# Kernel tuning notes

Hardware: AMD Instinct MI355X
Metric: run time of the kernel (lower is better)

Reference implementation:

```python
import jax, jax.numpy as jnp
import numpy as np

B = 8
C = 256
NS = [16384, 4096, 1024, 256, 1]  # point-pyramid sizes per level
D = 3                              # coordinate dim
EPS = (1e-06, 1e-06, 1e-06, 1e-06, 1e-06)


def _pm_level(x, coords_c, coords_n, idx, p_i, eps_i):
    """One hierarchical gather-weighted power-mean pooling step.
    x: (B, C, N)  coords_c: (B, N, D)  coords_n: (B, Nn, D)  idx: (B, N) in [0, Nn).
    Returns pooled features (B, C, Nn)."""
    Bq, Cq, N = x.shape
    Nn = coords_n.shape[1]
    Dd = coords_c.shape[-1]
    # gather parent coords for each child, delta to parent
    cn = jnp.take_along_axis(coords_n, idx[:, :, None], axis=1)            # (B,N,D)
    delta = coords_c - cn                                                   # (B,N,D)
    # per-parent max/min of delta (scatter_max / scatter_min)
    smax = jax.vmap(lambda d, ix: jax.ops.segment_max(d, ix, num_segments=Nn))(delta, idx)
    smin = jax.vmap(lambda d, ix: jax.ops.segment_min(d, ix, num_segments=Nn))(delta, idx)
    pos_ub = jnp.maximum(smax, 0.0)   # clamp(min=0)
    neg_lb = jnp.minimum(smin, 0.0)   # clamp(max=0)
    # gather bounds back to children, pick by sign of delta
    pos_g = jnp.take_along_axis(pos_ub, idx[:, :, None], axis=1)
    neg_g = jnp.take_along_axis(neg_lb, idx[:, :, None], axis=1)
    inuse = jnp.where(delta >= 0.0, pos_g, neg_g)
    w = 1.0 - jnp.abs(delta) / (jnp.abs(inuse) + 1e-6)                      # (B,N,D)
    # split channels across the D coordinate weights: [q, q, ..., q+r]
    q, r = Cq // Dd, Cq % Dd
    reps = np.asarray([q] * (Dd - 1) + [q + r])
    w_c = jnp.repeat(w, reps, axis=-1, total_repeat_length=Cq)              # (B,N,C)
    x_pow = jnp.maximum(x, eps_i) ** p_i                                    # (B,C,N)
    xw = x_pow.transpose(0, 2, 1) * w_c                                     # (B,N,C)
    # scatter_sum of weighted powers and of weights, per parent cell
    xw_s = jax.vmap(lambda a, ix: jax.ops.segment_sum(a, ix, num_segments=Nn))(xw, idx)   # (B,Nn,C)
    w_s = jax.vmap(lambda a, ix: jax.ops.segment_sum(a, ix, num_segments=Nn))(w_c, idx)   # (B,Nn,C)
    nxt = (xw_s / (w_s + 1e-6)) ** (1.0 / p_i)
    return nxt.transpose(0, 2, 1)                                           # (B,C,Nn)


def setup_inputs() -> dict:
    key = jax.random.key(0)
    ks = jax.random.split(key, 16)
    x = jax.random.normal(ks[0], (B, C, NS[0]), dtype=jnp.float32)
    coords = [jax.random.normal(ks[1 + i], (B, NS[i], D), dtype=jnp.float32) for i in range(5)]
    idxs = []
    for i in range(4):
        # every parent gets ~NS[i]/NS[i+1] children; permute per batch for irregular access
        base = jnp.arange(NS[i], dtype=jnp.int32) % NS[i + 1]
        bk = jax.random.split(ks[6 + i], B)
        idxs.append(jax.vmap(lambda k: jax.random.permutation(k, base))(bk))
    p = jnp.full((5,), 3.0, dtype=jnp.float32)
    return {"x": x,
            "idx0": idxs[0], "idx1": idxs[1], "idx2": idxs[2], "idx3": idxs[3],
            "coords0": coords[0], "coords1": coords[1], "coords2": coords[2],
            "coords3": coords[3], "coords4": coords[4],
            "p": p}


def reference(x, idx0, idx1, idx2, idx3, coords0, coords1, coords2, coords3, coords4, p):
    idxs = (idx0, idx1, idx2, idx3)
    coords = (coords0, coords1, coords2, coords3, coords4)
    cur = x
    for i in range(4):
        cur = _pm_level(cur, coords[i], coords[i + 1], idxs[i], p[i], EPS[i])
    return cur[..., 0]  # squeeze (B,C,1) -> (B,C)
```

## Files before the change

kernel.cpp:

```cpp
#include <hip/hip_runtime.h>
#include <math.h>

constexpr int B  = 8;
constexpr int C  = 256;
constexpr int Q  = 85;
constexpr int NS0 = 16384, NS1 = 4096, NS2 = 1024, NS3 = 256;
constexpr int PAR = NS1 + NS2 + NS3;
constexpr int SLT = NS0 + NS1 + NS2;

__device__ __forceinline__ int cdim(int c) {
    int d = c / Q;
    return d > 2 ? 2 : d;
}

__global__ void invert_fused_kernel(const int* __restrict__ idx0,
                                    const int* __restrict__ idx1,
                                    const int* __restrict__ idx2,
                                    const float* __restrict__ c0,
                                    const float* __restrict__ c1,
                                    const float* __restrict__ c2,
                                    const float* __restrict__ c3,
                                    const float* __restrict__ c4,
                                    unsigned* __restrict__ cnt,
                                    float4*   __restrict__ dslot,
                                    float*    __restrict__ w3,
                                    float*    __restrict__ z4) {
    __shared__ float sm[3][256];
    __shared__ float sn[3][256];

    if (blockIdx.y == 3) {
        if (blockIdx.x >= 8) return;
        int b = blockIdx.x;
        int n = threadIdx.x;

        float pc0 = c4[b * 3 + 0], pc1 = c4[b * 3 + 1], pc2 = c4[b * 3 + 2];
        const float* cp = &c3[((size_t)(b * 256 + n)) * 3];
        float d0 = cp[0] - pc0, d1 = cp[1] - pc1, d2 = cp[2] - pc2;
        sm[0][n] = d0; sm[1][n] = d1; sm[2][n] = d2;
        sn[0][n] = d0; sn[1][n] = d1; sn[2][n] = d2;
        __syncthreads();
        for (int s = 128; s > 0; s >>= 1) {
            if (n < s) {
#pragma unroll
                for (int d = 0; d < 3; ++d) {
                    sm[d][n] = fmaxf(sm[d][n], sm[d][n + s]);
                    sn[d][n] = fminf(sn[d][n], sn[d][n + s]);
                }
            }
            __syncthreads();
        }
        float pos0 = fmaxf(sm[0][0], 0.f), pos1 = fmaxf(sm[1][0], 0.f), pos2 = fmaxf(sm[2][0], 0.f);
        float neg0 = fminf(sn[0][0], 0.f), neg1 = fminf(sn[1][0], 0.f), neg2 = fminf(sn[2][0], 0.f);
        __syncthreads();

        float w0 = 1.f - fabsf(d0) / (fabsf(d0 >= 0.f ? pos0 : neg0) + 1e-6f);
        float w1 = 1.f - fabsf(d1) / (fabsf(d1 >= 0.f ? pos1 : neg1) + 1e-6f);
        float w2 = 1.f - fabsf(d2) / (fabsf(d2 >= 0.f ? pos2 : neg2) + 1e-6f);
        float* wp = &w3[((size_t)(b * 256 + n)) * 3];
        wp[0] = w0; wp[1] = w1; wp[2] = w2;

        sm[0][n] = w0; sm[1][n] = w1; sm[2][n] = w2;
        __syncthreads();
        for (int s = 128; s > 0; s >>= 1) {
            if (n < s) {
#pragma unroll
                for (int d = 0; d < 3; ++d) sm[d][n] += sm[d][n + s];
            }
            __syncthreads();
        }
        if (n == 0) {
            z4[b * 3 + 0] = sm[0][0];
            z4[b * 3 + 1] = sm[1][0];
            z4[b * 3 + 2] = sm[2][0];
        }
        return;
    }

    int lvl = blockIdx.y;
    const int*   idx = (lvl == 0) ? idx0 : (lvl == 1 ? idx1 : idx2);
    const float* cc  = (lvl == 0) ? c0   : (lvl == 1 ? c1   : c2);
    const float* cn  = (lvl == 0) ? c1   : (lvl == 1 ? c2   : c3);
    int N  = (lvl == 0) ? NS0 : (lvl == 1 ? NS1 : NS2);
    int Nn = (lvl == 0) ? NS1 : (lvl == 1 ? NS2 : NS3);
    int cbase = (lvl == 0) ? 0 : (lvl == 1 ? NS1 : NS1 + NS2);
    int sbase = (lvl == 0) ? 0 : (lvl == 1 ? NS0 : NS0 + NS1);

    int t = blockIdx.x * blockDim.x + threadIdx.x;
    if (t >= B * N) return;
    int b = t / N;
    int n = t - b * N;
    int j = idx[t];
    int pj = b * Nn + j;

    unsigned o = atomicAdd(&cnt[(size_t)b * PAR + cbase + j], 1u);
    int slot = (int)(o & 3u);

    float4 dv;
    dv.x = cc[(size_t)t * 3 + 0] - cn[(size_t)pj * 3 + 0];
    dv.y = cc[(size_t)t * 3 + 1] - cn[(size_t)pj * 3 + 1];
    dv.z = cc[(size_t)t * 3 + 2] - cn[(size_t)pj * 3 + 2];
    dv.w = __int_as_float(n);
    dslot[((size_t)b * SLT + sbase + (size_t)j * 4) + slot] = dv;
}

__global__ void weights_mid_kernel(const float4* __restrict__ dslot,
                                   float* __restrict__ w1,
                                   float* __restrict__ w2,
                                   float* __restrict__ z2,
                                   float* __restrict__ z3)
{
    int lvl = blockIdx.y + 1;
    int N  = (lvl == 1) ? NS1 : NS2;
    int Nn = (lvl == 1) ? NS2 : NS3;
    int sbase = (lvl == 1) ? NS0 : NS0 + NS1;
    float* w = (lvl == 1) ? w1 : w2;
    float* z = (lvl == 1) ? z2 : z3;

    int t = blockIdx.x * blockDim.x + threadIdx.x;
    if (t >= B * Nn) return;
    int b = t / Nn;
    int j = t - b * Nn;

    const float4* dp = &dslot[(size_t)b * SLT + sbase + (size_t)j * 4];
    float4 ch0 = dp[0], ch1 = dp[1], ch2 = dp[2], ch3 = dp[3];

    float mx0 = fmaxf(fmaxf(ch0.x, ch1.x), fmaxf(ch2.x, ch3.x));
    float mn0 = fminf(fminf(ch0.x, ch1.x), fminf(ch2.x, ch3.x));
    float mx1 = fmaxf(fmaxf(ch0.y, ch1.y), fmaxf(ch2.y, ch3.y));
    float mn1 = fminf(fminf(ch0.y, ch1.y), fminf(ch2.y, ch3.y));
    float mx2 = fmaxf(fmaxf(ch0.z, ch1.z), fmaxf(ch2.z, ch3.z));
    float mn2 = fminf(fminf(ch0.z, ch1.z), fminf(ch2.z, ch3.z));

    float pos0 = fmaxf(mx0, 0.f), neg0 = fminf(mn0, 0.f);
    float pos1 = fmaxf(mx1, 0.f), neg1 = fminf(mn1, 0.f);
    float pos2 = fmaxf(mx2, 0.f), neg2 = fminf(mn2, 0.f);

    float zz0 = 0.f, zz1 = 0.f, zz2 = 0.f;
    float4 chs[4] = {ch0, ch1, ch2, ch3};
#pragma unroll
    for (int k = 0; k < 4; ++k) {
        float d0 = chs[k].x, d1 = chs[k].y, d2 = chs[k].z;
        int   n  = __float_as_int(chs[k].w);
        float wv0 = 1.f - fabsf(d0) / (fabsf(d0 >= 0.f ? pos0 : neg0) + 1e-6f);
        float wv1 = 1.f - fabsf(d1) / (fabsf(d1 >= 0.f ? pos1 : neg1) + 1e-6f);
        float wv2 = 1.f - fabsf(d2) / (fabsf(d2 >= 0.f ? pos2 : neg2) + 1e-6f);
        float* wp = &w[((size_t)b * N + n) * 3];
        wp[0] = wv0; wp[1] = wv1; wp[2] = wv2;
        zz0 += wv0; zz1 += wv1; zz2 += wv2;
    }
    float* zp = &z[(size_t)t * 3];
    zp[0] = zz0; zp[1] = zz1; zp[2] = zz2;
}

__global__ void leafwn_kernel(const float4* __restrict__ dslot,
                              const int*   __restrict__ idx1,
                              const int*   __restrict__ idx2,
                              const float* __restrict__ w1,
                              const float* __restrict__ w2,
                              const float* __restrict__ w3,
                              const float* __restrict__ z2,
                              const float* __restrict__ z3,
                              const float* __restrict__ z4,
                              float* __restrict__ Wn) {
    int t = blockIdx.x * blockDim.x + threadIdx.x;
    if (t >= B * NS1) return;
    int b = t / NS1;
    int j = t - b * NS1;

    const float4* dp = &dslot[(size_t)b * SLT + (size_t)j * 4];
    float4 ch0 = dp[0], ch1 = dp[1], ch2 = dp[2], ch3 = dp[3];

    float mx0 = fmaxf(fmaxf(ch0.x, ch1.x), fmaxf(ch2.x, ch3.x));
    float mn0 = fminf(fminf(ch0.x, ch1.x), fminf(ch2.x, ch3.x));
    float mx1 = fmaxf(fmaxf(ch0.y, ch1.y), fmaxf(ch2.y, ch3.y));
    float mn1 = fminf(fminf(ch0.y, ch1.y), fminf(ch2.y, ch3.y));
    float mx2 = fmaxf(fmaxf(ch0.z, ch1.z), fmaxf(ch2.z, ch3.z));
    float mn2 = fminf(fminf(ch0.z, ch1.z), fminf(ch2.z, ch3.z));

    float pos0 = fmaxf(mx0, 0.f), neg0 = fminf(mn0, 0.f);
    float pos1 = fmaxf(mx1, 0.f), neg1 = fminf(mn1, 0.f);
    float pos2 = fmaxf(mx2, 0.f), neg2 = fminf(mn2, 0.f);

    float wv0[4], wv1[4], wv2[4];
    int   nid[4];
    float zz0 = 0.f, zz1 = 0.f, zz2 = 0.f;
    float4 chs[4] = {ch0, ch1, ch2, ch3};
#pragma unroll
    for (int k = 0; k < 4; ++k) {
        float d0 = chs[k].x, d1 = chs[k].y, d2 = chs[k].z;
        nid[k] = __float_as_int(chs[k].w);
        wv0[k] = 1.f - fabsf(d0) / (fabsf(d0 >= 0.f ? pos0 : neg0) + 1e-6f);
        wv1[k] = 1.f - fabsf(d1) / (fabsf(d1 >= 0.f ? pos1 : neg1) + 1e-6f);
        wv2[k] = 1.f - fabsf(d2) / (fabsf(d2 >= 0.f ? pos2 : neg2) + 1e-6f);
        zz0 += wv0[k]; zz1 += wv1[k]; zz2 += wv2[k];
    }

    int a2 = idx1[t];
    int a3 = idx2[(size_t)b * NS2 + a2];
    size_t i1 = (size_t)t * 3;
    size_t i2 = ((size_t)b * NS2 + a2) * 3;
    size_t i3 = ((size_t)b * NS3 + a3) * 3;
    float U0 = w1[i1 + 0] / (z2[i2 + 0] + 1e-6f) * w2[i2 + 0] / (z3[i3 + 0] + 1e-6f)
             * w3[i3 + 0] / (z4[b * 3 + 0] + 1e-6f);
    float U1v = w1[i1 + 1] / (z2[i2 + 1] + 1e-6f) * w2[i2 + 1] / (z3[i3 + 1] + 1e-6f)
             * w3[i3 + 1] / (z4[b * 3 + 1] + 1e-6f);
    float U2 = w1[i1 + 2] / (z2[i2 + 2] + 1e-6f) * w2[i2 + 2] / (z3[i3 + 2] + 1e-6f)
             * w3[i3 + 2] / (z4[b * 3 + 2] + 1e-6f);

    float r0 = U0 / (zz0 + 1e-6f);
    float r1 = U1v / (zz1 + 1e-6f);
    float r2 = U2 / (zz2 + 1e-6f);

    float* Wb0 = Wn + ((size_t)(b * 3 + 0)) * NS0;
    float* Wb1 = Wn + ((size_t)(b * 3 + 1)) * NS0;
    float* Wb2 = Wn + ((size_t)(b * 3 + 2)) * NS0;
#pragma unroll
    for (int k = 0; k < 4; ++k) {
        int n = nid[k];
        Wb0[n] = wv0[k] * r0;
        Wb1[n] = wv1[k] * r1;
        Wb2[n] = wv2[k] * r2;
    }
}

__global__ void final_kernel(const float* __restrict__ x,
                             const float* __restrict__ Wn,
                             float* __restrict__ out,
                             const float* __restrict__ p_arr) {
    __shared__ float sred[256];
    int bc = blockIdx.x;
    int b = bc / C;
    int c = bc - b * C;
    int d = cdim(c);
    float p = p_arr[0];
    bool p3 = (p == 3.0f);

    const float4* xr = (const float4*)(x + (size_t)bc * NS0);
    const float4* wr = (const float4*)(Wn + ((size_t)(b * 3 + d)) * NS0);

    float acc = 0.f;
#pragma unroll 8
    for (int i = threadIdx.x; i < NS0 / 4; i += 256) {
        float4 xv = xr[i];
        float4 wv = wr[i];
        float v0 = fmaxf(xv.x, 1e-6f);
        float v1 = fmaxf(xv.y, 1e-6f);
        float v2 = fmaxf(xv.z, 1e-6f);
        float v3 = fmaxf(xv.w, 1e-6f);
        float s0 = p3 ? v0 * v0 * v0 : powf(v0, p);
        float s1 = p3 ? v1 * v1 * v1 : powf(v1, p);
        float s2 = p3 ? v2 * v2 * v2 : powf(v2, p);
        float s3 = p3 ? v3 * v3 * v3 : powf(v3, p);
        acc = fmaf(s0, wv.x, acc);
        acc = fmaf(s1, wv.y, acc);
        acc = fmaf(s2, wv.z, acc);
        acc = fmaf(s3, wv.w, acc);
    }
    sred[threadIdx.x] = acc;
    __syncthreads();
    for (int s = 128; s > 0; s >>= 1) {
        if (threadIdx.x < s) sred[threadIdx.x] += sred[threadIdx.x + s];
        __syncthreads();
    }
    if (threadIdx.x == 0) {
        float t = sred[0];
        out[bc] = p3 ? cbrtf(t) : powf(t, 1.0f / p);
    }
}

extern "C" void kernel_launch(void* const* d_in, const int* in_sizes, int n_in,
                              void* d_out, int out_size, void* d_ws, size_t ws_size,
                              hipStream_t stream) {
    const float* x      = (const float*)d_in[0];
    const int*   idx0   = (const int*)d_in[1];
    const int*   idx1   = (const int*)d_in[2];
    const int*   idx2   = (const int*)d_in[3];
    const float* coords0 = (const float*)d_in[5];
    const float* coords1 = (const float*)d_in[6];
    const float* coords2 = (const float*)d_in[7];
    const float* coords3 = (const float*)d_in[8];
    const float* coords4 = (const float*)d_in[9];
    const float* p = (const float*)d_in[10];

    char* ws = (char*)d_ws;
    size_t off = 0;
    auto alloc = [&](size_t bytes) -> void* {
        off = (off + 255) & ~(size_t)255;
        void* r = ws + off;
        off += bytes;
        return r;
    };

    unsigned* cnt  = (unsigned*)alloc((size_t)B * PAR * sizeof(unsigned));
    float4*  dslot = (float4*)alloc((size_t)B * SLT * sizeof(float4));
    float* w1 = (float*)alloc((size_t)B * NS1 * 3 * sizeof(float));
    float* w2 = (float*)alloc((size_t)B * NS2 * 3 * sizeof(float));
    float* w3 = (float*)alloc((size_t)B * NS3 * 3 * sizeof(float));
    float* z2 = (float*)alloc((size_t)B * NS2 * 3 * sizeof(float));
    float* z3 = (float*)alloc((size_t)B * NS3 * 3 * sizeof(float));
    float* z4 = (float*)alloc((size_t)B * 1   * 3 * sizeof(float));
    float* Wn = (float*)alloc((size_t)B * 3 * NS0 * sizeof(float));

    dim3 ig((B * NS0 + 255) / 256, 4);
    invert_fused_kernel<<<ig, 256, 0, stream>>>(
        idx0, idx1, idx2, coords0, coords1, coords2, coords3, coords4,
        cnt, dslot, w3, z4);

    dim3 mg((B * NS2 + 255) / 256, 2);
    weights_mid_kernel<<<mg, 256, 0, stream>>>(dslot, w1, w2, z2, z3);

    leafwn_kernel<<<(B * NS1 + 255) / 256, 256, 0, stream>>>(
        dslot, idx1, idx2, w1, w2, w3, z2, z3, z4, Wn);

    final_kernel<<<B * C, 256, 0, stream>>>(x, Wn, (float*)d_out, p);
}
```

Measured before the change: 50.86 us.

## Merge weight-precompute kernels into one cooperative kernel with grid sync

Replaces the three weight-building kernels (invert, mid-level weights, leaf Wn) with a single cooperative kernel using a grid-wide barrier between the scatter phase and the leaf phase. The mid-level weights and normalizers are no longer stored; each leaf thread recomputes its ancestor's sibling weights from the slot buffer. This removes two kernel launches and the intermediate w1/w2/z2/z3 buffers, at the cost of redundant per-leaf ancestor recomputation and a grid.sync on a fixed 512-block grid.

```diff
diff --git a/kernel.cpp b/kernel.cpp
--- a/kernel.cpp
+++ b/kernel.cpp
@@ -1,5 +1,8 @@
 #include <hip/hip_runtime.h>
+#include <hip/hip_cooperative_groups.h>
 #include <math.h>
+
+namespace cg = cooperative_groups;
 
 constexpr int B  = 8;
 constexpr int C  = 256;
@@ -7,34 +10,63 @@
 constexpr int NS0 = 16384, NS1 = 4096, NS2 = 1024, NS3 = 256;
 constexpr int PAR = NS1 + NS2 + NS3;
 constexpr int SLT = NS0 + NS1 + NS2;
+constexpr int GRID_W = 512;
 
 __device__ __forceinline__ int cdim(int c) {
     int d = c / Q;
     return d > 2 ? 2 : d;
 }
 
-__global__ void invert_fused_kernel(const int* __restrict__ idx0,
-                                    const int* __restrict__ idx1,
-                                    const int* __restrict__ idx2,
-                                    const float* __restrict__ c0,
-                                    const float* __restrict__ c1,
-                                    const float* __restrict__ c2,
-                                    const float* __restrict__ c3,
-                                    const float* __restrict__ c4,
-                                    unsigned* __restrict__ cnt,
-                                    float4*   __restrict__ dslot,
-                                    float*    __restrict__ w3,
-                                    float*    __restrict__ z4) {
+struct CP {
+    const int   *idx0, *idx1, *idx2;
+    const float *c0, *c1, *c2, *c3, *c4;
+    unsigned    *cnt;
+    float4      *dslot;
+    float       *w3;
+    float       *z4;
+    float       *Wn;
+};
+
+__device__ __forceinline__ void sib_w(float4 c0, float4 c1, float4 c2, float4 c3,
+                                      int target,
+                                      float& wt0, float& wt1, float& wt2,
+                                      float& zs0, float& zs1, float& zs2) {
+    float mx0 = fmaxf(fmaxf(c0.x, c1.x), fmaxf(c2.x, c3.x));
+    float mn0 = fminf(fminf(c0.x, c1.x), fminf(c2.x, c3.x));
+    float mx1 = fmaxf(fmaxf(c0.y, c1.y), fmaxf(c2.y, c3.y));
+    float mn1 = fminf(fminf(c0.y, c1.y), fminf(c2.y, c3.y));
+    float mx2 = fmaxf(fmaxf(c0.z, c1.z), fmaxf(c2.z, c3.z));
+    float mn2 = fminf(fminf(c0.z, c1.z), fminf(c2.z, c3.z));
+    float pos0 = fmaxf(mx0, 0.f), neg0 = fminf(mn0, 0.f);
+    float pos1 = fmaxf(mx1, 0.f), neg1 = fminf(mn1, 0.f);
+    float pos2 = fmaxf(mx2, 0.f), neg2 = fminf(mn2, 0.f);
+
+    zs0 = zs1 = zs2 = 0.f;
+    wt0 = wt1 = wt2 = 0.f;
+    float4 chs[4] = {c0, c1, c2, c3};
+#pragma unroll
+    for (int k = 0; k < 4; ++k) {
+        float d0 = chs[k].x, d1 = chs[k].y, d2 = chs[k].z;
+        int   n  = __float_as_int(chs[k].w);
+        float wv0 = 1.f - fabsf(d0) / (fabsf(d0 >= 0.f ? pos0 : neg0) + 1e-6f);
+        float wv1 = 1.f - fabsf(d1) / (fabsf(d1 >= 0.f ? pos1 : neg1) + 1e-6f);
+        float wv2 = 1.f - fabsf(d2) / (fabsf(d2 >= 0.f ? pos2 : neg2) + 1e-6f);
+        zs0 += wv0; zs1 += wv1; zs2 += wv2;
+        if (n == target) { wt0 = wv0; wt1 = wv1; wt2 = wv2; }
+    }
+}
+
+__global__ __launch_bounds__(256)
+void weights_coop_kernel(CP P) {
     __shared__ float sm[3][256];
     __shared__ float sn[3][256];
-
-    if (blockIdx.y == 3) {
-        if (blockIdx.x >= 8) return;
+    cg::grid_group grid = cg::this_grid();
+
+    if (blockIdx.x < 8) {
         int b = blockIdx.x;
         int n = threadIdx.x;
-
-        float pc0 = c4[b * 3 + 0], pc1 = c4[b * 3 + 1], pc2 = c4[b * 3 + 2];
-        const float* cp = &c3[((size_t)(b * 256 + n)) * 3];
+        float pc0 = P.c4[b * 3 + 0], pc1 = P.c4[b * 3 + 1], pc2 = P.c4[b * 3 + 2];
+        const float* cp = &P.c3[((size_t)(b * 256 + n)) * 3];
         float d0 = cp[0] - pc0, d1 = cp[1] - pc1, d2 = cp[2] - pc2;
         sm[0][n] = d0; sm[1][n] = d1; sm[2][n] = d2;
         sn[0][n] = d0; sn[1][n] = d1; sn[2][n] = d2;
@@ -56,7 +88,7 @@
         float w0 = 1.f - fabsf(d0) / (fabsf(d0 >= 0.f ? pos0 : neg0) + 1e-6f);
         float w1 = 1.f - fabsf(d1) / (fabsf(d1 >= 0.f ? pos1 : neg1) + 1e-6f);
         float w2 = 1.f - fabsf(d2) / (fabsf(d2 >= 0.f ? pos2 : neg2) + 1e-6f);
-        float* wp = &w3[((size_t)(b * 256 + n)) * 3];
+        float* wp = &P.w3[((size_t)(b * 256 + n)) * 3];
         wp[0] = w0; wp[1] = w1; wp[2] = w2;
 
         sm[0][n] = w0; sm[1][n] = w1; sm[2][n] = w2;
@@ -69,157 +101,102 @@
             __syncthreads();
         }
         if (n == 0) {
-            z4[b * 3 + 0] = sm[0][0];
-            z4[b * 3 + 1] = sm[1][0];
-            z4[b * 3 + 2] = sm[2][0];
-        }
-        return;
-    }
-
-    int lvl = blockIdx.y;
-    const int*   idx = (lvl == 0) ? idx0 : (lvl == 1 ? idx1 : idx2);
-    const float* cc  = (lvl == 0) ? c0   : (lvl == 1 ? c1   : c2);
-    const float* cn  = (lvl == 0) ? c1   : (lvl == 1 ? c2   : c3);
-    int N  = (lvl == 0) ? NS0 : (lvl == 1 ? NS1 : NS2);
-    int Nn = (lvl == 0) ? NS1 : (lvl == 1 ? NS2 : NS3);
-    int cbase = (lvl == 0) ? 0 : (lvl == 1 ? NS1 : NS1 + NS2);
-    int sbase = (lvl == 0) ? 0 : (lvl == 1 ? NS0 : NS0 + NS1);
-
-    int t = blockIdx.x * blockDim.x + threadIdx.x;
-    if (t >= B * N) return;
-    int b = t / N;
-    int n = t - b * N;
-    int j = idx[t];
-    int pj = b * Nn + j;
-
-    unsigned o = atomicAdd(&cnt[(size_t)b * PAR + cbase + j], 1u);
-    int slot = (int)(o & 3u);
-
-    float4 dv;
-    dv.x = cc[(size_t)t * 3 + 0] - cn[(size_t)pj * 3 + 0];
-    dv.y = cc[(size_t)t * 3 + 1] - cn[(size_t)pj * 3 + 1];
-    dv.z = cc[(size_t)t * 3 + 2] - cn[(size_t)pj * 3 + 2];
-    dv.w = __int_as_float(n);
-    dslot[((size_t)b * SLT + sbase + (size_t)j * 4) + slot] = dv;
-}
-
-__global__ void weights_mid_kernel(const float4* __restrict__ dslot,
-                                   float* __restrict__ w1,
-                                   float* __restrict__ w2,
-                                   float* __restrict__ z2,
-                                   float* __restrict__ z3)
-{
-    int lvl = blockIdx.y + 1;
-    int N  = (lvl == 1) ? NS1 : NS2;
-    int Nn = (lvl == 1) ? NS2 : NS3;
-    int sbase = (lvl == 1) ? NS0 : NS0 + NS1;
-    float* w = (lvl == 1) ? w1 : w2;
-    float* z = (lvl == 1) ? z2 : z3;
-
-    int t = blockIdx.x * blockDim.x + threadIdx.x;
-    if (t >= B * Nn) return;
-    int b = t / Nn;
-    int j = t - b * Nn;
-
-    const float4* dp = &dslot[(size_t)b * SLT + sbase + (size_t)j * 4];
-    float4 ch0 = dp[0], ch1 = dp[1], ch2 = dp[2], ch3 = dp[3];
-
-    float mx0 = fmaxf(fmaxf(ch0.x, ch1.x), fmaxf(ch2.x, ch3.x));
-    float mn0 = fminf(fminf(ch0.x, ch1.x), fminf(ch2.x, ch3.x));
-    float mx1 = fmaxf(fmaxf(ch0.y, ch1.y), fmaxf(ch2.y, ch3.y));
-    float mn1 = fminf(fminf(ch0.y, ch1.y), fminf(ch2.y, ch3.y));
-    float mx2 = fmaxf(fmaxf(ch0.z, ch1.z), fmaxf(ch2.z, ch3.z));
-    float mn2 = fminf(fminf(ch0.z, ch1.z), fminf(ch2.z, ch3.z));
-
-    float pos0 = fmaxf(mx0, 0.f), neg0 = fminf(mn0, 0.f);
-    float pos1 = fmaxf(mx1, 0.f), neg1 = fminf(mn1, 0.f);
-    float pos2 = fmaxf(mx2, 0.f), neg2 = fminf(mn2, 0.f);
-
-    float zz0 = 0.f, zz1 = 0.f, zz2 = 0.f;
-    float4 chs[4] = {ch0, ch1, ch2, ch3};
-#pragma unroll
-    for (int k = 0; k < 4; ++k) {
-        float d0 = chs[k].x, d1 = chs[k].y, d2 = chs[k].z;
-        int   n  = __float_as_int(chs[k].w);
-        float wv0 = 1.f - fabsf(d0) / (fabsf(d0 >= 0.f ? pos0 : neg0) + 1e-6f);
-        float wv1 = 1.f - fabsf(d1) / (fabsf(d1 >= 0.f ? pos1 : neg1) + 1e-6f);
-        float wv2 = 1.f - fabsf(d2) / (fabsf(d2 >= 0.f ? pos2 : neg2) + 1e-6f);
-        float* wp = &w[((size_t)b * N + n) * 3];
-        wp[0] = wv0; wp[1] = wv1; wp[2] = wv2;
-        zz0 += wv0; zz1 += wv1; zz2 += wv2;
-    }
-    float* zp = &z[(size_t)t * 3];
-    zp[0] = zz0; zp[1] = zz1; zp[2] = zz2;
-}
-
-__global__ void leafwn_kernel(const float4* __restrict__ dslot,
-                              const int*   __restrict__ idx1,
-                              const int*   __restrict__ idx2,
-                              const float* __restrict__ w1,
-                              const float* __restrict__ w2,
-                              const float* __restrict__ w3,
-                              const float* __restrict__ z2,
-                              const float* __restrict__ z3,
-                              const float* __restrict__ z4,
-                              float* __restrict__ Wn) {
-    int t = blockIdx.x * blockDim.x + threadIdx.x;
-    if (t >= B * NS1) return;
-    int b = t / NS1;
-    int j = t - b * NS1;
-
-    const float4* dp = &dslot[(size_t)b * SLT + (size_t)j * 4];
-    float4 ch0 = dp[0], ch1 = dp[1], ch2 = dp[2], ch3 = dp[3];
-
-    float mx0 = fmaxf(fmaxf(ch0.x, ch1.x), fmaxf(ch2.x, ch3.x));
-    float mn0 = fminf(fminf(ch0.x, ch1.x), fminf(ch2.x, ch3.x));
-    float mx1 = fmaxf(fmaxf(ch0.y, ch1.y), fmaxf(ch2.y, ch3.y));
-    float mn1 = fminf(fminf(ch0.y, ch1.y), fminf(ch2.y, ch3.y));
-    float mx2 = fmaxf(fmaxf(ch0.z, ch1.z), fmaxf(ch2.z, ch3.z));
-    float mn2 = fminf(fminf(ch0.z, ch1.z), fminf(ch2.z, ch3.z));
-
-    float pos0 = fmaxf(mx0, 0.f), neg0 = fminf(mn0, 0.f);
-    float pos1 = fmaxf(mx1, 0.f), neg1 = fminf(mn1, 0.f);
-    float pos2 = fmaxf(mx2, 0.f), neg2 = fminf(mn2, 0.f);
-
-    float wv0[4], wv1[4], wv2[4];
-    int   nid[4];
-    float zz0 = 0.f, zz1 = 0.f, zz2 = 0.f;
-    float4 chs[4] = {ch0, ch1, ch2, ch3};
-#pragma unroll
-    for (int k = 0; k < 4; ++k) {
-        float d0 = chs[k].x, d1 = chs[k].y, d2 = chs[k].z;
-        nid[k] = __float_as_int(chs[k].w);
-        wv0[k] = 1.f - fabsf(d0) / (fabsf(d0 >= 0.f ? pos0 : neg0) + 1e-6f);
-        wv1[k] = 1.f - fabsf(d1) / (fabsf(d1 >= 0.f ? pos1 : neg1) + 1e-6f);
-        wv2[k] = 1.f - fabsf(d2) / (fabsf(d2 >= 0.f ? pos2 : neg2) + 1e-6f);
-        zz0 += wv0[k]; zz1 += wv1[k]; zz2 += wv2[k];
-    }
-
-    int a2 = idx1[t];
-    int a3 = idx2[(size_t)b * NS2 + a2];
-    size_t i1 = (size_t)t * 3;
-    size_t i2 = ((size_t)b * NS2 + a2) * 3;
-    size_t i3 = ((size_t)b * NS3 + a3) * 3;
-    float U0 = w1[i1 + 0] / (z2[i2 + 0] + 1e-6f) * w2[i2 + 0] / (z3[i3 + 0] + 1e-6f)
-             * w3[i3 + 0] / (z4[b * 3 + 0] + 1e-6f);
-    float U1v = w1[i1 + 1] / (z2[i2 + 1] + 1e-6f) * w2[i2 + 1] / (z3[i3 + 1] + 1e-6f)
-             * w3[i3 + 1] / (z4[b * 3 + 1] + 1e-6f);
-    float U2 = w1[i1 + 2] / (z2[i2 + 2] + 1e-6f) * w2[i2 + 2] / (z3[i3 + 2] + 1e-6f)
-             * w3[i3 + 2] / (z4[b * 3 + 2] + 1e-6f);
-
-    float r0 = U0 / (zz0 + 1e-6f);
-    float r1 = U1v / (zz1 + 1e-6f);
-    float r2 = U2 / (zz2 + 1e-6f);
-
-    float* Wb0 = Wn + ((size_t)(b * 3 + 0)) * NS0;
-    float* Wb1 = Wn + ((size_t)(b * 3 + 1)) * NS0;
-    float* Wb2 = Wn + ((size_t)(b * 3 + 2)) * NS0;
-#pragma unroll
-    for (int k = 0; k < 4; ++k) {
-        int n = nid[k];
-        Wb0[n] = wv0[k] * r0;
-        Wb1[n] = wv1[k] * r1;
-        Wb2[n] = wv2[k] * r2;
+            P.z4[b * 3 + 0] = sm[0][0];
+            P.z4[b * 3 + 1] = sm[1][0];
+            P.z4[b * 3 + 2] = sm[2][0];
+        }
+    }
+
+    {
+        const int u0 = B * NS0;
+        const int u1 = u0 + B * NS1;
+        const int utot = u1 + B * NS2;
+        for (int u = blockIdx.x * 256 + threadIdx.x; u < utot; u += GRID_W * 256) {
+            const int* idx; const float *cc, *cn;
+            int N, Nn, cbase, sbase, v;
+            if (u < u0)      { v = u;      idx = P.idx0; cc = P.c0; cn = P.c1; N = NS0; Nn = NS1; cbase = 0;         sbase = 0; }
+            else if (u < u1) { v = u - u0; idx = P.idx1; cc = P.c1; cn = P.c2; N = NS1; Nn = NS2; cbase = NS1;       sbase = NS0; }
+            else             { v = u - u1; idx = P.idx2; cc = P.c2; cn = P.c3; N = NS2; Nn = NS3; cbase = NS1 + NS2; sbase = NS0 + NS1; }
+            int b = v / N;
+            int n = v - b * N;
+            int j = idx[(size_t)b * N + n];
+            int pj = b * Nn + j;
+
+            unsigned o = atomicAdd(&P.cnt[(size_t)b * PAR + cbase + j], 1u);
+            int slot = (int)(o & 3u);
+
+            float4 dv;
+            dv.x = cc[((size_t)b * N + n) * 3 + 0] - cn[(size_t)pj * 3 + 0];
+            dv.y = cc[((size_t)b * N + n) * 3 + 1] - cn[(size_t)pj * 3 + 1];
+            dv.z = cc[((size_t)b * N + n) * 3 + 2] - cn[(size_t)pj * 3 + 2];
+            dv.w = __int_as_float(n);
+            P.dslot[((size_t)b * SLT + sbase + (size_t)j * 4) + slot] = dv;
+        }
+    }
+
+    __threadfence();
+    grid.sync();
+
+    for (int t = blockIdx.x * 256 + threadIdx.x; t < B * NS1; t += GRID_W * 256) {
+        int b = t / NS1;
+        int j = t - b * NS1;
+
+        const float4* dp0 = &P.dslot[(size_t)b * SLT + (size_t)j * 4];
+        float4 l0 = dp0[0], l1 = dp0[1], l2 = dp0[2], l3 = dp0[3];
+
+        float mx0 = fmaxf(fmaxf(l0.x, l1.x), fmaxf(l2.x, l3.x));
+        float mn0 = fminf(fminf(l0.x, l1.x), fminf(l2.x, l3.x));
+        float mx1 = fmaxf(fmaxf(l0.y, l1.y), fmaxf(l2.y, l3.y));
+        float mn1 = fminf(fminf(l0.y, l1.y), fminf(l2.y, l3.y));
+        float mx2 = fmaxf(fmaxf(l0.z, l1.z), fmaxf(l2.z, l3.z));
+        float mn2 = fminf(fminf(l0.z, l1.z), fminf(l2.z, l3.z));
+        float pos0 = fmaxf(mx0, 0.f), neg0 = fminf(mn0, 0.f);
+        float pos1 = fmaxf(mx1, 0.f), neg1 = fminf(mn1, 0.f);
+        float pos2 = fmaxf(mx2, 0.f), neg2 = fminf(mn2, 0.f);
+
+        float wv0[4], wv1[4], wv2[4];
+        int   nid[4];
+        float zz0 = 0.f, zz1 = 0.f, zz2 = 0.f;
+        float4 chs[4] = {l0, l1, l2, l3};
+#pragma unroll
+        for (int k = 0; k < 4; ++k) {
+            float d0 = chs[k].x, d1 = chs[k].y, d2 = chs[k].z;
+            nid[k] = __float_as_int(chs[k].w);
+            wv0[k] = 1.f - fabsf(d0) / (fabsf(d0 >= 0.f ? pos0 : neg0) + 1e-6f);
+            wv1[k] = 1.f - fabsf(d1) / (fabsf(d1 >= 0.f ? pos1 : neg1) + 1e-6f);
+            wv2[k] = 1.f - fabsf(d2) / (fabsf(d2 >= 0.f ? pos2 : neg2) + 1e-6f);
+            zz0 += wv0[k]; zz1 += wv1[k]; zz2 += wv2[k];
+        }
+
+        int a2 = P.idx1[(size_t)b * NS1 + j];
+        const float4* dp1 = &P.dslot[(size_t)b * SLT + NS0 + (size_t)a2 * 4];
+        float w1t0, w1t1, w1t2, z20, z21, z22;
+        sib_w(dp1[0], dp1[1], dp1[2], dp1[3], j, w1t0, w1t1, w1t2, z20, z21, z22);
+
+        int a3 = P.idx2[(size_t)b * NS2 + a2];
+        const float4* dp2 = &P.dslot[(size_t)b * SLT + NS0 + NS1 + (size_t)a3 * 4];
+        float w2t0, w2t1, w2t2, z30, z31, z32;
+        sib_w(dp2[0], dp2[1], dp2[2], dp2[3], a2, w2t0, w2t1, w2t2, z30, z31, z32);
+
+        const float* w3p = &P.w3[((size_t)b * 256 + a3) * 3];
+        float U0 = w1t0 / (z20 + 1e-6f) * w2t0 / (z30 + 1e-6f) * w3p[0] / (P.z4[b * 3 + 0] + 1e-6f);
+        float U1 = w1t1 / (z21 + 1e-6f) * w2t1 / (z31 + 1e-6f) * w3p[1] / (P.z4[b * 3 + 1] + 1e-6f);
+        float U2 = w1t2 / (z22 + 1e-6f) * w2t2 / (z32 + 1e-6f) * w3p[2] / (P.z4[b * 3 + 2] + 1e-6f);
+
+        float r0 = U0 / (zz0 + 1e-6f);
+        float r1 = U1 / (zz1 + 1e-6f);
+        float r2 = U2 / (zz2 + 1e-6f);
+
+        float* Wb0 = P.Wn + ((size_t)(b * 3 + 0)) * NS0;
+        float* Wb1 = P.Wn + ((size_t)(b * 3 + 1)) * NS0;
+        float* Wb2 = P.Wn + ((size_t)(b * 3 + 2)) * NS0;
+#pragma unroll
+        for (int k = 0; k < 4; ++k) {
+            int n = nid[k];
+            Wb0[n] = wv0[k] * r0;
+            Wb1[n] = wv1[k] * r1;
+            Wb2[n] = wv2[k] * r2;
+        }
     }
 }
 
@@ -293,24 +270,18 @@
 
     unsigned* cnt  = (unsigned*)alloc((size_t)B * PAR * sizeof(unsigned));
     float4*  dslot = (float4*)alloc((size_t)B * SLT * sizeof(float4));
-    float* w1 = (float*)alloc((size_t)B * NS1 * 3 * sizeof(float));
-    float* w2 = (float*)alloc((size_t)B * NS2 * 3 * sizeof(float));
     float* w3 = (float*)alloc((size_t)B * NS3 * 3 * sizeof(float));
-    float* z2 = (float*)alloc((size_t)B * NS2 * 3 * sizeof(float));
-    float* z3 = (float*)alloc((size_t)B * NS3 * 3 * sizeof(float));
     float* z4 = (float*)alloc((size_t)B * 1   * 3 * sizeof(float));
     float* Wn = (float*)alloc((size_t)B * 3 * NS0 * sizeof(float));
 
-    dim3 ig((B * NS0 + 255) / 256, 4);
-    invert_fused_kernel<<<ig, 256, 0, stream>>>(
-        idx0, idx1, idx2, coords0, coords1, coords2, coords3, coords4,
-        cnt, dslot, w3, z4);
-
-    dim3 mg((B * NS2 + 255) / 256, 2);
-    weights_mid_kernel<<<mg, 256, 0, stream>>>(dslot, w1, w2, z2, z3);
-
-    leafwn_kernel<<<(B * NS1 + 255) / 256, 256, 0, stream>>>(
-        dslot, idx1, idx2, w1, w2, w3, z2, z3, z4, Wn);
+    CP P;
+    P.idx0 = idx0; P.idx1 = idx1; P.idx2 = idx2;
+    P.c0 = coords0; P.c1 = coords1; P.c2 = coords2; P.c3 = coords3; P.c4 = coords4;
+    P.cnt = cnt; P.dslot = dslot; P.w3 = w3; P.z4 = z4; P.Wn = Wn;
+
+    void* args[] = { &P };
+    hipLaunchCooperativeKernel((const void*)weights_coop_kernel,
+                               dim3(GRID_W), dim3(256), args, 0, stream);
 
     final_kernel<<<B * C, 256, 0, stream>>>(x, Wn, (float*)d_out, p);
 }
```

Measured after the change: 184.1 us. 262% more time.
